# Kernel tuning notes

Measured on AMD Instinct MI355X. Metric: run time of the kernel, lower is better.

Reference implementation:

```python
import jax, jax.numpy as jnp
import numpy as np

N = 100000
E = 1600000
IN_C = 128
HID = 256
K_EIG = 64
OUT_C = 16


def setup_inputs() -> dict:
    key = jax.random.key(0)
    ks = jax.random.split(key, 8)
    x = jax.random.normal(ks[0], (N, IN_C), dtype=jnp.float32)
    edge_index = jax.random.randint(ks[1], (2, E), 0, N)
    MLP_W = jax.random.normal(ks[2], (K_EIG, N), dtype=jnp.float32) * 0.02
    MLP_b = jax.random.normal(ks[3], (K_EIG,), dtype=jnp.float32) * 0.02
    mlpx_W = jax.random.normal(ks[4], (HID, IN_C), dtype=jnp.float32) * 0.05
    mlpx_b = jax.random.normal(ks[5], (HID,), dtype=jnp.float32) * 0.02
    fin_W = jax.random.normal(ks[6], (OUT_C, HID + K_EIG), dtype=jnp.float32) * 0.05
    fin_b = jax.random.normal(ks[7], (OUT_C,), dtype=jnp.float32) * 0.02
    return {"x": x, "edge_index": edge_index, "MLP_W": MLP_W, "MLP_b": MLP_b,
            "mlpx_W": mlpx_W, "mlpx_b": mlpx_b, "fin_W": fin_W, "fin_b": fin_b}


def _spmm(row, col, feats, n):
    # adj is COO with coords (col[e], row[e]) and value 1 -> out[col] += feats[row]
    return jax.ops.segment_sum(feats[row], col, num_segments=n)


def _pump(xA, row, col, n):
    # MinCut-style pump: soft assignment, normalized-cut loss + orthogonality loss
    S = jax.nn.softmax(xA, axis=-1)                      # [N, K]
    AS = _spmm(row, col, S, n)                            # A @ S, [N, K]
    cut = jnp.sum(S * AS)                                 # tr(S^T A S)
    deg = jax.ops.segment_sum(jnp.ones(col.shape, S.dtype), col, num_segments=n)
    deg_term = jnp.sum(deg[:, None] * S * S)              # tr(S^T D S)
    pump_loss = -(cut / deg_term)
    SS = S.T @ S                                          # [K, K]
    k = S.shape[1]
    ortho_loss = jnp.linalg.norm(SS / jnp.linalg.norm(SS)
                                 - jnp.eye(k, dtype=S.dtype) / jnp.sqrt(jnp.asarray(k, S.dtype)))
    return S, pump_loss, ortho_loss


def reference(x, edge_index, MLP_W, MLP_b, mlpx_W, mlpx_b, fin_W, fin_b):
    row, col = edge_index[0], edge_index[1]
    n = x.shape[0]
    # xA = adj @ MLP.weight.T + bias   (irregular gather/scatter over edges)
    xA = _spmm(row, col, MLP_W.T, n) + MLP_b              # [N, K]
    xX = x @ mlpx_W.T + mlpx_b                            # [N, HID]
    xA, pump_loss, ortho_loss = _pump(xA, row, col, n)
    z = jnp.concatenate([xX, xA], axis=1)                 # [N, HID+K]
    # dropout omitted (eval mode)
    z = jax.nn.log_softmax(z @ fin_W.T + fin_b, axis=-1)  # [N, OUT]
    return (z, pump_loss + ortho_loss)
```

## Files before the change

### kernel.cpp

```cpp
#include <hip/hip_runtime.h>
#include <math.h>

#define N_NODES 100000
#define N_EDGES 1600000
#define IN_C    128
#define HID     256
#define KEIG    64
#define OUT_C   16

#define NPB      256
#define NBUCKET  ((N_NODES + NPB - 1) / NPB)
#define EDGE_TILE 2048
#define NTILE    ((N_EDGES + EDGE_TILE - 1) / EDGE_TILE)
#define CAP      8960

#define TRANS_BLOCKS   ((N_NODES + 63) / 64)
#define GATHER_BLOCKS  ((N_NODES + 63) / 64)
#define CUT_VB         1582
#define SSP_BLOCKS     226
#define SSP_ALLOC      256
#define OUTG_BLOCKS    226
#define TAIL_BLOCKS    (113 * 18)

typedef __attribute__((ext_vector_type(8))) short short8;
typedef __attribute__((ext_vector_type(4))) float f32x4;
typedef __attribute__((ext_vector_type(2))) float f32x2;

__device__ __forceinline__ float wave_sum(float v) {
#pragma unroll
    for (int m = 32; m; m >>= 1) v += __shfl_xor(v, m, 64);
    return v;
}
__device__ __forceinline__ float bf2f(unsigned int u) {
    return __uint_as_float((u & 0xffffu) << 16);
}
__device__ __forceinline__ unsigned short f2bf(float f) {
    unsigned int u = __float_as_uint(f);
    u += 0x7fff + ((u >> 16) & 1);
    return (unsigned short)(u >> 16);
}
__device__ __forceinline__ unsigned char f2fp8(float f) {
    int p = __builtin_amdgcn_cvt_pk_fp8_f32(f, f, 0, false);
    return (unsigned char)(p & 0xff);
}

#define FMA4(P, s, W) \
    P.x = fmaf(s, W.x, P.x); P.y = fmaf(s, W.y, P.y); \
    P.z = fmaf(s, W.z, P.z); P.w = fmaf(s, W.w, P.w);

#define GLD(TBL, R) (*(const unsigned*)((TBL) + (unsigned)(R) * 64u + cb))

#define CONS4(ACC) do { f32x2 p_;                                                   \
    p_ = __builtin_amdgcn_cvt_pk_f32_fp8(uA0, false); ACC.x += p_.x; ACC.y += p_.y; \
    p_ = __builtin_amdgcn_cvt_pk_f32_fp8(uA0, true);  ACC.z += p_.x; ACC.w += p_.y; \
    p_ = __builtin_amdgcn_cvt_pk_f32_fp8(uA1, false); ACC.x += p_.x; ACC.y += p_.y; \
    p_ = __builtin_amdgcn_cvt_pk_f32_fp8(uA1, true);  ACC.z += p_.x; ACC.w += p_.y; \
    p_ = __builtin_amdgcn_cvt_pk_f32_fp8(uA2, false); ACC.x += p_.x; ACC.y += p_.y; \
    p_ = __builtin_amdgcn_cvt_pk_f32_fp8(uA2, true);  ACC.z += p_.x; ACC.w += p_.y; \
    p_ = __builtin_amdgcn_cvt_pk_f32_fp8(uA3, false); ACC.x += p_.x; ACC.y += p_.y; \
    p_ = __builtin_amdgcn_cvt_pk_f32_fp8(uA3, true);  ACC.z += p_.x; ACC.w += p_.y; \
} while (0)

__global__ void prep_weff(const float* __restrict__ mlpxW, const float* __restrict__ mlpxb,
                          const float* __restrict__ finW, const float* __restrict__ finb,
                          float* __restrict__ Weff, float* __restrict__ beff,
                          int* __restrict__ bcnt, unsigned char* __restrict__ WT8,
                          unsigned char* __restrict__ S8, int* __restrict__ gpad) {
    int t = blockIdx.x * blockDim.x + threadIdx.x;
    const int NW = (IN_C + KEIG) * OUT_C;
    if (t < NW) {
        int k = t >> 4, o = t & 15;
        float acc;
        if (k < IN_C) {
            acc = 0.f;
            for (int c = 0; c < HID; ++c)
                acc += mlpxW[c * IN_C + k] * finW[o * (HID + KEIG) + c];
        } else {
            acc = finW[o * (HID + KEIG) + HID + (k - IN_C)];
        }
        Weff[k * OUT_C + o] = acc;
    }
    int tb = t - NW;
    if (tb >= 0 && tb < OUT_C) {
        float acc = finb[tb];
        for (int c = 0; c < HID; ++c) acc += mlpxb[c] * finW[tb * (HID + KEIG) + c];
        beff[tb] = acc;
    }
    int tz = t - (NW + OUT_C);
    if (tz >= 0 && tz <= NBUCKET) bcnt[tz] = 0;
    int tp = t - (NW + OUT_C + NBUCKET + 1);
    if (tp >= 0 && tp < 16) {
        ((int*)(WT8 + (size_t)N_NODES * 64))[tp] = 0;
        ((int*)(S8 + (size_t)N_NODES * 64))[tp] = 0;
        if (tp == 0) *gpad = 0;
    }
}

__global__ __launch_bounds__(256) void fused_prep(const float* __restrict__ W,
                                                  unsigned char* __restrict__ WT8,
                                                  const int* __restrict__ ei,
                                                  int* __restrict__ bcnt) {
    __shared__ __align__(16) char sm[64 * 65 * 4];
    int t = threadIdx.x;
    if (blockIdx.x < TRANS_BLOCKS) {
        float (*tile)[65] = (float (*)[65])sm;
        int n0 = blockIdx.x * 64;
        int tn = t & 63, tq = t >> 6;
#pragma unroll
        for (int kk = 0; kk < 16; ++kk) {
            int k = tq * 16 + kk;
            int n = n0 + tn;
            tile[k][tn] = (n < N_NODES) ? W[(long long)k * N_NODES + n] : 0.f;
        }
        __syncthreads();
        int tk = t & 63;
#pragma unroll
        for (int ii = 0; ii < 16; ++ii) {
            int n = n0 + tq * 16 + ii;
            if (n < N_NODES) WT8[(unsigned)n * 64u + tk] = f2fp8(tile[tk][tq * 16 + ii] * 32.f);
        }
    } else {
        int* h = (int*)sm;
        for (int i = t; i < NBUCKET; i += 256) h[i] = 0;
        __syncthreads();
        int tile_i = blockIdx.x - TRANS_BLOCKS;
        int e0 = tile_i * EDGE_TILE;
        int e1 = min(e0 + EDGE_TILE, N_EDGES);
        for (int e = e0 + t; e < e1; e += 256)
            atomicAdd(&h[ei[N_EDGES + e] >> 8], 1);
        __syncthreads();
        for (int i = t; i < NBUCKET; i += 256)
            if (h[i]) atomicAdd(&bcnt[i], h[i]);
    }
}

__global__ void bucket_scan(const int* __restrict__ bcnt, int* __restrict__ bbase,
                            int* __restrict__ bcur) {
    __shared__ int sh[512];
    int t = threadIdx.x;
    int v = (t < NBUCKET) ? bcnt[t] : 0;
    sh[t] = v;
    __syncthreads();
    for (int d = 1; d < 512; d <<= 1) {
        int u = (t >= d) ? sh[t - d] : 0;
        __syncthreads();
        sh[t] += u;
        __syncthreads();
    }
    if (t < NBUCKET) { bbase[t] = sh[t] - v; bcur[t] = sh[t] - v; }
    if (t == 0) bbase[NBUCKET] = N_EDGES;
}

__global__ void bucket_scatter(const int* __restrict__ ei, int* __restrict__ bcur,
                               int* __restrict__ ebuf) {
    __shared__ int h[NBUCKET];
    __shared__ int gb[NBUCKET];
    __shared__ int lpre[NBUCKET];
    __shared__ int psum[256];
    __shared__ int stage[EDGE_TILE];
    __shared__ short bkt[EDGE_TILE];
    int t = threadIdx.x;
    for (int i = t; i < NBUCKET; i += 256) h[i] = 0;
    __syncthreads();
    int e0 = blockIdx.x * EDGE_TILE;
    int e1 = min(e0 + EDGE_TILE, N_EDGES);
    int nt = e1 - e0;
    for (int e = e0 + t; e < e1; e += 256)
        atomicAdd(&h[ei[N_EDGES + e] >> 8], 1);
    __syncthreads();
    int a0 = (2 * t < NBUCKET) ? h[2 * t] : 0;
    int a1 = (2 * t + 1 < NBUCKET) ? h[2 * t + 1] : 0;
    psum[t] = a0 + a1;
    __syncthreads();
    for (int d = 1; d < 256; d <<= 1) {
        int u = (t >= d) ? psum[t - d] : 0;
        __syncthreads();
        psum[t] += u;
        __syncthreads();
    }
    int base = (t == 0) ? 0 : psum[t - 1];
    if (2 * t < NBUCKET) lpre[2 * t] = base;
    if (2 * t + 1 < NBUCKET) lpre[2 * t + 1] = base + a0;
    __syncthreads();
    for (int i = t; i < NBUCKET; i += 256) {
        int c = h[i];
        gb[i] = c ? atomicAdd(&bcur[i], c) : 0;
        h[i] = lpre[i];
    }
    __syncthreads();
    for (int e = e0 + t; e < e1; e += 256) {
        int r = ei[e];
        int c = ei[N_EDGES + e];
        int b = c >> 8;
        int slot = atomicAdd(&h[b], 1);
        stage[slot] = r | ((c & 255) << 17);
        bkt[slot] = (short)b;
    }
    __syncthreads();
    for (int s = t; s < nt; s += 256) {
        int b = bkt[s];
        ebuf[gb[b] + s - lpre[b]] = stage[s];
    }
}

__global__ void csr_build(const int* __restrict__ ebuf, const int* __restrict__ bbase,
                          int2* __restrict__ nodei,
                          int* __restrict__ csr_row, int* __restrict__ gpad) {
    __shared__ int hist[NPB];
    __shared__ int sh[NPB];
    __shared__ int curs[NPB];
    __shared__ int staged[CAP];
    __shared__ int pbase_sh;
    int b = blockIdx.x;
    int t = threadIdx.x;
    int s0 = bbase[b], s1 = bbase[b + 1];
    hist[t] = 0;
    __syncthreads();
    for (int i = s0 + t; i < s1; i += 256)
        atomicAdd(&hist[ebuf[i] >> 17], 1);
    __syncthreads();
    int v = hist[t];
    int pv = (v + 15) & ~15;
    sh[t] = pv;
    __syncthreads();
    for (int d = 1; d < 256; d <<= 1) {
        int u = (t >= d) ? sh[t - d] : 0;
        __syncthreads();
        sh[t] += u;
        __syncthreads();
    }
    int pexcl = sh[t] - pv;
    int pt = sh[255];
    if (t == 0) pbase_sh = atomicAdd(gpad, pt);
    __syncthreads();
    int pbase = pbase_sh;
    int node = b * NPB + t;
    if (node < N_NODES) nodei[node] = make_int2(v, pbase + pexcl);
    curs[t] = pexcl;
    __syncthreads();
    if (pt <= CAP) {
        for (int i = t; i < pt; i += 256) staged[i] = N_NODES;
        __syncthreads();
        for (int i = s0 + t; i < s1; i += 256) {
            int pk = ebuf[i];
            int pos = atomicAdd(&curs[pk >> 17], 1);
            staged[pos] = pk & 0x1FFFF;
        }
        __syncthreads();
        for (int i = t; i < pt; i += 256) csr_row[pbase + i] = staged[i];
    } else {
        for (int i = t; i < pt; i += 256) csr_row[pbase + i] = N_NODES;
        __syncthreads();
        for (int i = s0 + t; i < s1; i += 256) {
            int pk = ebuf[i];
            int pos = atomicAdd(&curs[pk >> 17], 1);
            csr_row[pbase + pos] = pk & 0x1FFFF;
        }
    }
}

__global__ __launch_bounds__(256, 4) void gather_softmax(
        const int2* __restrict__ nodei, const int* __restrict__ csr_row,
        const unsigned char* __restrict__ WT8, const float* __restrict__ MLPb,
        unsigned short* __restrict__ Sb, unsigned char* __restrict__ S8,
        float* __restrict__ dtp) {
    int lane = threadIdx.x & 63;
    int q = lane >> 4;
    int c = lane & 15;
    unsigned cb = (unsigned)c * 4u;
    int wib = __builtin_amdgcn_readfirstlane(threadIdx.x >> 6);
    int n0 = (blockIdx.x * 4 + wib) * 16;
    float dacc = 0.f;
    if (n0 < N_NODES) {
        int nvalid = min(16, N_NODES - n0);
        int2 di = nodei[n0 + min(c, nvalid - 1)];
        f32x4 bias = *(const f32x4*)(MLPb + c * 4);
        int ps0  = __shfl(di.y, 0, 64);
        int degL = __shfl(di.x, nvalid - 1, 64);
        int psL  = __shfl(di.y, nvalid - 1, 64);
        int G = ((psL + ((degL + 15) & ~15)) - ps0) >> 4;
        const int* cw = csr_row + ps0 + (q << 2);
        int4 iB = {0, 0, 0, 0};
        unsigned uA0 = 0, uA1 = 0, uA2 = 0, uA3 = 0;
        if (G > 0) {
            int4 iA = *(const int4*)(cw);
            uA0 = GLD(WT8, iA.x); uA1 = GLD(WT8, iA.y);
            uA2 = GLD(WT8, iA.z); uA3 = GLD(WT8, iA.w);
            int g1 = (G > 1) ? 1 : 0;
            iB = *(const int4*)(cw + (g1 << 4));
        }
        int g = 0;
        for (int k = 0; k < nvalid; ++k) {
            int deg = __shfl(di.x, k, 64);
            int gcnt = (deg + 15) >> 4;
            f32x4 acc = {0.f, 0.f, 0.f, 0.f};
            for (int tt = 0; tt < gcnt; ++tt) {
                int gn = g + 2; if (gn >= G) gn = G - 1;
                int4 iC = *(const int4*)(cw + (gn << 4));
                unsigned uB0 = GLD(WT8, iB.x);
                unsigned uB1 = GLD(WT8, iB.y);
                unsigned uB2 = GLD(WT8, iB.z);
                unsigned uB3 = GLD(WT8, iB.w);
                CONS4(acc);
                uA0 = uB0; uA1 = uB1; uA2 = uB2; uA3 = uB3; iB = iC;
                ++g;
            }
#pragma unroll
            for (int mm = 16; mm < 64; mm <<= 1) {
                acc.x += __shfl_xor(acc.x, mm, 64);
                acc.y += __shfl_xor(acc.y, mm, 64);
                acc.z += __shfl_xor(acc.z, mm, 64);
                acc.w += __shfl_xor(acc.w, mm, 64);
            }
            float ax = bias.x + acc.x * 0.03125f;
            float ay = bias.y + acc.y * 0.03125f;
            float az = bias.z + acc.z * 0.03125f;
            float aw = bias.w + acc.w * 0.03125f;
            float m4 = fmaxf(fmaxf(ax, ay), fmaxf(az, aw));
#pragma unroll
            for (int mm = 1; mm < 16; mm <<= 1) m4 = fmaxf(m4, __shfl_xor(m4, mm, 64));
            float ex = __expf(ax - m4), ey = __expf(ay - m4);
            float ez = __expf(az - m4), ew = __expf(aw - m4);
            float s4 = (ex + ey) + (ez + ew);
#pragma unroll
            for (int mm = 1; mm < 16; mm <<= 1) s4 += __shfl_xor(s4, mm, 64);
            float inv = 1.f / s4;
            float sx = ex * inv, sy = ey * inv, sz = ez * inv, sw = ew * inv;
            if (q == 0) {
                unsigned nidx = (unsigned)(n0 + k);
                unsigned lo = (unsigned)f2bf(sx) | ((unsigned)f2bf(sy) << 16);
                unsigned hi = (unsigned)f2bf(sz) | ((unsigned)f2bf(sw) << 16);
                *(uint2*)(Sb + nidx * 64u + cb) = make_uint2(lo, hi);
                int p8 = __builtin_amdgcn_cvt_pk_fp8_f32(sx * 64.f, sy * 64.f, 0, false);
                p8 = __builtin_amdgcn_cvt_pk_fp8_f32(sz * 64.f, sw * 64.f, p8, true);
                *(unsigned*)(S8 + nidx * 64u + cb) = (unsigned)p8;
            }
            dacc += (float)deg * ((sx * sx + sy * sy) + (sz * sz + sw * sw));
        }
    }
    dacc = wave_sum(dacc);
    __shared__ float red[4];
    if (lane == 0) red[wib] = dacc * 0.25f;
    __syncthreads();
    if (threadIdx.x == 0) dtp[blockIdx.x] = red[0] + red[1] + red[2] + red[3];
}

__global__ __launch_bounds__(256, 8) void fused_tail(
        const int2* __restrict__ nodei,
        const int* __restrict__ csr_row,
        const unsigned short* __restrict__ Sb, const unsigned char* __restrict__ S8,
        float* __restrict__ cutp, float* __restrict__ ssp,
        const float* __restrict__ x, const float* __restrict__ Weff,
        const float* __restrict__ beff, float* __restrict__ out) {
    __shared__ __align__(16) char sm[768 * 16 + 64];
    int t = threadIdx.x;
    int grp = blockIdx.x / 18;
    int r18 = blockIdx.x % 18;

    if (r18 < 14) {
        int vb = grp * 14 + r18;
        int lane = t & 63;
        int q = lane >> 4;
        int c = lane & 15;
        unsigned cb = (unsigned)c * 4u;
        int wib = __builtin_amdgcn_readfirstlane(t >> 6);
        int n0 = vb * 64 + wib * 16;
        float cacc = 0.f;
        if (n0 < N_NODES) {
            int nvalid = min(16, N_NODES - n0);
            int2 di = nodei[n0 + min(c, nvalid - 1)];
            int ps0  = __shfl(di.y, 0, 64);
            int degL = __shfl(di.x, nvalid - 1, 64);
            int psL  = __shfl(di.y, nvalid - 1, 64);
            int G = ((psL + ((degL + 15) & ~15)) - ps0) >> 4;
            const int* cw = csr_row + ps0 + (q << 2);
            uint2 suA = *(const uint2*)(Sb + (unsigned)n0 * 64u + cb);
            unsigned uA0 = 0, uA1 = 0, uA2 = 0, uA3 = 0;
            unsigned uB0 = 0, uB1 = 0, uB2 = 0, uB3 = 0;
            int4 iC = {0, 0, 0, 0};
            int4 iD = {0, 0, 0, 0};
            if (G > 0) {
                int4 i0 = *(const int4*)(cw);
                uA0 = GLD(S8, i0.x); uA1 = GLD(S8, i0.y);
                uA2 = GLD(S8, i0.z); uA3 = GLD(S8, i0.w);
                int g1 = (G > 1) ? 1 : G - 1;
                int4 i1 = *(const int4*)(cw + (g1 << 4));
                uB0 = GLD(S8, i1.x); uB1 = GLD(S8, i1.y);
                uB2 = GLD(S8, i1.z); uB3 = GLD(S8, i1.w);
                int g2 = (G > 2) ? 2 : G - 1;
                iC = *(const int4*)(cw + (g2 << 4));
                int g3 = (G > 3) ? 3 : G - 1;
                iD = *(const int4*)(cw + (g3 << 4));
            }
            int g = 0;
            for (int k = 0; k < nvalid; ++k) {
                int deg = __shfl(di.x, k, 64);
                int gcnt = (deg + 15) >> 4;
                uint2 suN = *(const uint2*)(Sb + (unsigned)(n0 + min(k + 1, nvalid - 1)) * 64u + cb);
                f32x4 acc = {0.f, 0.f, 0.f, 0.f};
                for (int tt = 0; tt < gcnt; ++tt) {
                    int gn = g + 4; if (gn >= G) gn = G - 1;
                    int4 iE_ = *(const int4*)(cw + (gn << 4));
                    unsigned uC0_ = GLD(S8, iC.x), uC1_ = GLD(S8, iC.y);
                    unsigned uC2_ = GLD(S8, iC.z), uC3_ = GLD(S8, iC.w);
                    CONS4(acc);
                    uA0 = uB0; uA1 = uB1; uA2 = uB2; uA3 = uB3;
                    uB0 = uC0_; uB1 = uC1_; uB2 = uC2_; uB3 = uC3_;
                    iC = iD; iD = iE_;
                    ++g;
                }
                cacc += bf2f(suA.x) * acc.x + bf2f(suA.x >> 16) * acc.y
                      + bf2f(suA.y) * acc.z + bf2f(suA.y >> 16) * acc.w;
                suA = suN;
            }
        }
        cacc = wave_sum(cacc);
        float* red = (float*)sm;
        if (lane == 0) red[wib] = cacc * 0.015625f;
        __syncthreads();
        if (t == 0) cutp[vb] = red[0] + red[1] + red[2] + red[3];
    } else if (r18 < 16) {
        int bid2 = grp * 2 + (r18 - 14);
        unsigned short (*Sr)[66] = (unsigned short (*)[66])sm;
        int lane = t & 63;
        int w = t >> 6;
        int m = lane & 15;
        int quad = lane >> 4;
        int srow = t >> 3;
        int spart = t & 7;
        f32x4 a0 = {0.f,0.f,0.f,0.f}, a1 = {0.f,0.f,0.f,0.f};
        f32x4 a2 = {0.f,0.f,0.f,0.f}, a3 = {0.f,0.f,0.f,0.f};
        for (int base = bid2 * 32; base < N_NODES; base += SSP_BLOCKS * 32) {
            const uint4* g = (const uint4*)(Sb + (long long)(base + srow) * 64 + spart * 8);
            uint4 d = *g;
            __syncthreads();
            unsigned int* rowp = (unsigned int*)&Sr[srow][0];
            rowp[spart * 4 + 0] = d.x;
            rowp[spart * 4 + 1] = d.y;
            rowp[spart * 4 + 2] = d.z;
            rowp[spart * 4 + 3] = d.w;
            __syncthreads();
            short8 f0, f1, f2, f3;
#pragma unroll
            for (int j = 0; j < 8; ++j) {
                int k = quad * 8 + j;
                f0[j] = (short)Sr[k][m];
                f1[j] = (short)Sr[k][16 + m];
                f2[j] = (short)Sr[k][32 + m];
                f3[j] = (short)Sr[k][48 + m];
            }
            short8 fa = (w == 0) ? f0 : (w == 1) ? f1 : (w == 2) ? f2 : f3;
            a0 = __builtin_amdgcn_mfma_f32_16x16x32_bf16(fa, f0, a0, 0, 0, 0);
            a1 = __builtin_amdgcn_mfma_f32_16x16x32_bf16(fa, f1, a1, 0, 0, 0);
            a2 = __builtin_amdgcn_mfma_f32_16x16x32_bf16(fa, f2, a2, 0, 0, 0);
            a3 = __builtin_amdgcn_mfma_f32_16x16x32_bf16(fa, f3, a3, 0, 0, 0);
        }
        float* dst = ssp + (size_t)bid2 * 4096;
#pragma unroll
        for (int r = 0; r < 4; ++r) {
            int row = w * 16 + quad * 4 + r;
            dst[row * 64 +  0 + m] = a0[r];
            dst[row * 64 + 16 + m] = a1[r];
            dst[row * 64 + 32 + m] = a2[r];
            dst[row * 64 + 48 + m] = a3[r];
        }
    } else {
        int obid = grp * 2 + (r18 - 16);
        float4* Wsh = (float4*)sm;
        float* bsh = (float*)(sm + 768 * 16);
        const float4* W4 = (const float4*)Weff;
        for (int i = t; i < 768; i += 256) Wsh[i] = W4[i];
        if (t < 16) bsh[t] = beff[t];
        __syncthreads();
        for (int r = obid * 256 + t; r < N_NODES; r += OUTG_BLOCKS * 256) {
            float4 p0 = make_float4(bsh[0], bsh[1], bsh[2], bsh[3]);
            float4 p1 = make_float4(bsh[4], bsh[5], bsh[6], bsh[7]);
            float4 p2 = make_float4(bsh[8], bsh[9], bsh[10], bsh[11]);
            float4 p3 = make_float4(bsh[12], bsh[13], bsh[14], bsh[15]);
            const float4* xr = (const float4*)(x + (long long)r * IN_C);
#pragma unroll 8
            for (int j = 0; j < 32; ++j) {
                float4 xv = xr[j];
                int k = j * 4;
                float xs[4] = {xv.x, xv.y, xv.z, xv.w};
#pragma unroll
                for (int c = 0; c < 4; ++c) {
                    float s = xs[c];
                    float4 w0 = Wsh[(k + c) * 4 + 0];
                    float4 w1 = Wsh[(k + c) * 4 + 1];
                    float4 w2 = Wsh[(k + c) * 4 + 2];
                    float4 w3 = Wsh[(k + c) * 4 + 3];
                    FMA4(p0, s, w0); FMA4(p1, s, w1); FMA4(p2, s, w2); FMA4(p3, s, w3);
                }
            }
            const uint2* sr = (const uint2*)(Sb + (long long)r * 64);
#pragma unroll 8
            for (int j = 0; j < 16; ++j) {
                uint2 u = sr[j];
                float xs[4] = {bf2f(u.x), bf2f(u.x >> 16), bf2f(u.y), bf2f(u.y >> 16)};
                int k = IN_C + j * 4;
#pragma unroll
                for (int c = 0; c < 4; ++c) {
                    float s = xs[c];
                    float4 w0 = Wsh[(k + c) * 4 + 0];
                    float4 w1 = Wsh[(k + c) * 4 + 1];
                    float4 w2 = Wsh[(k + c) * 4 + 2];
                    float4 w3 = Wsh[(k + c) * 4 + 3];
                    FMA4(p0, s, w0); FMA4(p1, s, w1); FMA4(p2, s, w2); FMA4(p3, s, w3);
                }
            }
            float m = fmaxf(fmaxf(fmaxf(p0.x, p0.y), fmaxf(p0.z, p0.w)),
                            fmaxf(fmaxf(fmaxf(p1.x, p1.y), fmaxf(p1.z, p1.w)),
                                  fmaxf(fmaxf(fmaxf(p2.x, p2.y), fmaxf(p2.z, p2.w)),
                                        fmaxf(fmaxf(p3.x, p3.y), fmaxf(p3.z, p3.w)))));
            float sum = __expf(p0.x - m) + __expf(p0.y - m) + __expf(p0.z - m) + __expf(p0.w - m)
                      + __expf(p1.x - m) + __expf(p1.y - m) + __expf(p1.z - m) + __expf(p1.w - m)
                      + __expf(p2.x - m) + __expf(p2.y - m) + __expf(p2.z - m) + __expf(p2.w - m)
                      + __expf(p3.x - m) + __expf(p3.y - m) + __expf(p3.z - m) + __expf(p3.w - m);
            float lse = m + logf(sum);
            float4* o4 = (float4*)(out + (long long)r * OUT_C);
            o4[0] = make_float4(p0.x - lse, p0.y - lse, p0.z - lse, p0.w - lse);
            o4[1] = make_float4(p1.x - lse, p1.y - lse, p1.z - lse, p1.w - lse);
            o4[2] = make_float4(p2.x - lse, p2.y - lse, p2.z - lse, p2.w - lse);
            o4[3] = make_float4(p3.x - lse, p3.y - lse, p3.z - lse, p3.w - lse);
        }
    }
}

__global__ void reduce_ss(const float* __restrict__ ssp, float* __restrict__ SS) {
    int e = blockIdx.x * blockDim.x + threadIdx.x;
    float s = 0.f;
    for (int p = 0; p < SSP_BLOCKS; ++p) s += ssp[(size_t)p * 4096 + e];
    SS[e] = s;
}

__global__ void scalars_kernel(const float* __restrict__ cutp, const float* __restrict__ dtp,
                               const float* __restrict__ SS, float* __restrict__ out) {
    __shared__ float red[256];
    int t = threadIdx.x;
    float c = 0.f;
    for (int i = t; i < CUT_VB; i += 256) c += cutp[i];
    red[t] = c; __syncthreads();
    for (int s = 128; s; s >>= 1) { if (t < s) red[t] += red[t + s]; __syncthreads(); }
    float cut = red[0]; __syncthreads();

    float d = 0.f;
    for (int i = t; i < GATHER_BLOCKS; i += 256) d += dtp[i];
    red[t] = d; __syncthreads();
    for (int s = 128; s; s >>= 1) { if (t < s) red[t] += red[t + s]; __syncthreads(); }
    float dterm = red[0]; __syncthreads();

    float ss[16];
    float sq = 0.f;
#pragma unroll
    for (int j = 0; j < 16; ++j) { ss[j] = SS[t * 16 + j]; sq += ss[j] * ss[j]; }
    red[t] = sq; __syncthreads();
    for (int s = 128; s; s >>= 1) { if (t < s) red[t] += red[t + s]; __syncthreads(); }
    float nrm = sqrtf(red[0]); __syncthreads();

    float osq = 0.f;
#pragma unroll
    for (int j = 0; j < 16; ++j) {
        int idx = t * 16 + j;
        float v = ss[j] / nrm - ((idx % 65 == 0) ? 0.125f : 0.f);
        osq += v * v;
    }
    red[t] = osq; __syncthreads();
    for (int s = 128; s; s >>= 1) { if (t < s) red[t] += red[t + s]; __syncthreads(); }
    if (t == 0) {
        float loss = -(cut / dterm) + sqrtf(red[0]);
        out[(long long)N_NODES * OUT_C] = loss;
    }
}

extern "C" void kernel_launch(void* const* d_in, const int* in_sizes, int n_in,
                              void* d_out, int out_size, void* d_ws, size_t ws_size,
                              hipStream_t stream) {
    const float* x     = (const float*)d_in[0];
    const int*   ei    = (const int*)d_in[1];
    const float* MLPW  = (const float*)d_in[2];
    const float* MLPb  = (const float*)d_in[3];
    const float* mlpxW = (const float*)d_in[4];
    const float* mlpxb = (const float*)d_in[5];
    const float* finW  = (const float*)d_in[6];
    const float* finb  = (const float*)d_in[7];
    float* out = (float*)d_out;
    char* ws = (char*)d_ws;

    unsigned char*  WT8 = (unsigned char*)ws;
    unsigned char*  S8  = (unsigned char*)(ws + (size_t)(N_NODES + 1) * 64);
    unsigned short* Sb  = (unsigned short*)(ws + (size_t)(N_NODES + 1) * 128);
    char* p = ws + (size_t)(N_NODES + 1) * 128 + (size_t)N_NODES * 128;
    float* ssp  = (float*)p;
    float* SS   = ssp + (size_t)SSP_ALLOC * 4096;
    float* Weff = SS + 4096;
    float* beff = Weff + 192 * 16;
    float* cutp = beff + 16;
    float* dtp  = cutp + 2048;
    int* ebuf    = (int*)(dtp + 2048);
    int* csr_row = ebuf + N_EDGES;
    int2* nodei  = (int2*)(csr_row + N_EDGES + 16 * N_NODES);
    int* bcnt    = (int*)(nodei + N_NODES);
    int* bbase   = bcnt + NBUCKET + 1;
    int* bcur    = bbase + NBUCKET + 1;
    int* gpad    = bcur + NBUCKET;

    hipLaunchKernelGGL(prep_weff, dim3(16), dim3(256), 0, stream,
                       mlpxW, mlpxb, finW, finb, Weff, beff, bcnt, WT8, S8, gpad);
    hipLaunchKernelGGL(fused_prep, dim3(TRANS_BLOCKS + NTILE), dim3(256), 0, stream,
                       MLPW, WT8, ei, bcnt);
    hipLaunchKernelGGL(bucket_scan, dim3(1), dim3(512), 0, stream, bcnt, bbase, bcur);
    hipLaunchKernelGGL(bucket_scatter, dim3(NTILE), dim3(256), 0, stream, ei, bcur, ebuf);
    hipLaunchKernelGGL(csr_build, dim3(NBUCKET), dim3(256), 0, stream,
                       ebuf, bbase, nodei, csr_row, gpad);
    hipLaunchKernelGGL(gather_softmax, dim3(GATHER_BLOCKS), dim3(256), 0, stream,
                       nodei, csr_row, WT8, MLPb, Sb, S8, dtp);
    hipLaunchKernelGGL(fused_tail, dim3(TAIL_BLOCKS), dim3(256), 0, stream,
                       nodei, csr_row, Sb, S8, cutp, ssp, x, Weff, beff, out);
    hipLaunchKernelGGL(reduce_ss, dim3(16), dim3(256), 0, stream, ssp, SS);
    hipLaunchKernelGGL(scalars_kernel, dim3(1), dim3(256), 0, stream, cutp, dtp, SS, out);
}
```

Before: 324.3 us.

## Fuse CSR build with gather-softmax, halve bucket size, read indices from LDS

Merges the CSR construction kernel and the gather+softmax kernel into one per-bucket kernel. The padded row indices staged in shared memory are reused directly for the WT8 gather instead of being reread from global memory. Buckets shrink from 256 to 128 nodes so the staging array fits within the occupancy bound, and the scan and scatter kernels are resized to match. This removes one launch and the global reread of csr_row, at the cost of giving up the cross-node software prefetch pipeline and possibly leaving less parallelism per block.

```diff
diff --git a/kernel.cpp b/kernel.cpp
--- a/kernel.cpp
+++ b/kernel.cpp
@@ -8,14 +8,13 @@
 #define KEIG    64
 #define OUT_C   16
 
-#define NPB      256
+#define NPB      128
 #define NBUCKET  ((N_NODES + NPB - 1) / NPB)
 #define EDGE_TILE 2048
 #define NTILE    ((N_EDGES + EDGE_TILE - 1) / EDGE_TILE)
-#define CAP      8960
+#define CAP      4608
 
 #define TRANS_BLOCKS   ((N_NODES + 63) / 64)
-#define GATHER_BLOCKS  ((N_NODES + 63) / 64)
 #define CUT_VB         1582
 #define SSP_BLOCKS     226
 #define SSP_ALLOC      256
@@ -59,6 +58,20 @@
     p_ = __builtin_amdgcn_cvt_pk_f32_fp8(uA2, true);  ACC.z += p_.x; ACC.w += p_.y; \
     p_ = __builtin_amdgcn_cvt_pk_f32_fp8(uA3, false); ACC.x += p_.x; ACC.y += p_.y; \
     p_ = __builtin_amdgcn_cvt_pk_f32_fp8(uA3, true);  ACC.z += p_.x; ACC.w += p_.y; \
+} while (0)
+
+#define GS_GATHER(IDX4, ACC) do {                                                   \
+    int4 ii_ = IDX4(0);                                                             \
+    unsigned uA0 = GLD(WT8, ii_.x), uA1 = GLD(WT8, ii_.y);                          \
+    unsigned uA2 = GLD(WT8, ii_.z), uA3 = GLD(WT8, ii_.w);                          \
+    for (int j_ = 16; j_ < plen; j_ += 16) {                                        \
+        int4 jj_ = IDX4(j_);                                                        \
+        unsigned uB0 = GLD(WT8, jj_.x), uB1 = GLD(WT8, jj_.y);                      \
+        unsigned uB2 = GLD(WT8, jj_.z), uB3 = GLD(WT8, jj_.w);                      \
+        CONS4(ACC);                                                                 \
+        uA0 = uB0; uA1 = uB1; uA2 = uB2; uA3 = uB3;                                 \
+    }                                                                               \
+    CONS4(ACC);                                                                     \
 } while (0)
 
 __global__ void prep_weff(const float* __restrict__ mlpxW, const float* __restrict__ mlpxb,
@@ -127,7 +140,7 @@
         int e0 = tile_i * EDGE_TILE;
         int e1 = min(e0 + EDGE_TILE, N_EDGES);
         for (int e = e0 + t; e < e1; e += 256)
-            atomicAdd(&h[ei[N_EDGES + e] >> 8], 1);
+            atomicAdd(&h[ei[N_EDGES + e] >> 7], 1);
         __syncthreads();
         for (int i = t; i < NBUCKET; i += 256)
             if (h[i]) atomicAdd(&bcnt[i], h[i]);
@@ -136,12 +149,12 @@
 
 __global__ void bucket_scan(const int* __restrict__ bcnt, int* __restrict__ bbase,
                             int* __restrict__ bcur) {
-    __shared__ int sh[512];
+    __shared__ int sh[1024];
     int t = threadIdx.x;
     int v = (t < NBUCKET) ? bcnt[t] : 0;
     sh[t] = v;
     __syncthreads();
-    for (int d = 1; d < 512; d <<= 1) {
+    for (int d = 1; d < 1024; d <<= 1) {
         int u = (t >= d) ? sh[t - d] : 0;
         __syncthreads();
         sh[t] += u;
@@ -166,11 +179,13 @@
     int e1 = min(e0 + EDGE_TILE, N_EDGES);
     int nt = e1 - e0;
     for (int e = e0 + t; e < e1; e += 256)
-        atomicAdd(&h[ei[N_EDGES + e] >> 8], 1);
-    __syncthreads();
-    int a0 = (2 * t < NBUCKET) ? h[2 * t] : 0;
-    int a1 = (2 * t + 1 < NBUCKET) ? h[2 * t + 1] : 0;
-    psum[t] = a0 + a1;
+        atomicAdd(&h[ei[N_EDGES + e] >> 7], 1);
+    __syncthreads();
+    int a0 = (4 * t + 0 < NBUCKET) ? h[4 * t + 0] : 0;
+    int a1 = (4 * t + 1 < NBUCKET) ? h[4 * t + 1] : 0;
+    int a2 = (4 * t + 2 < NBUCKET) ? h[4 * t + 2] : 0;
+    int a3 = (4 * t + 3 < NBUCKET) ? h[4 * t + 3] : 0;
+    psum[t] = a0 + a1 + a2 + a3;
     __syncthreads();
     for (int d = 1; d < 256; d <<= 1) {
         int u = (t >= d) ? psum[t - d] : 0;
@@ -179,8 +194,10 @@
         __syncthreads();
     }
     int base = (t == 0) ? 0 : psum[t - 1];
-    if (2 * t < NBUCKET) lpre[2 * t] = base;
-    if (2 * t + 1 < NBUCKET) lpre[2 * t + 1] = base + a0;
+    if (4 * t + 0 < NBUCKET) lpre[4 * t + 0] = base;
+    if (4 * t + 1 < NBUCKET) lpre[4 * t + 1] = base + a0;
+    if (4 * t + 2 < NBUCKET) lpre[4 * t + 2] = base + a0 + a1;
+    if (4 * t + 3 < NBUCKET) lpre[4 * t + 3] = base + a0 + a1 + a2;
     __syncthreads();
     for (int i = t; i < NBUCKET; i += 256) {
         int c = h[i];
@@ -191,9 +208,9 @@
     for (int e = e0 + t; e < e1; e += 256) {
         int r = ei[e];
         int c = ei[N_EDGES + e];
-        int b = c >> 8;
+        int b = c >> 7;
         int slot = atomicAdd(&h[b], 1);
-        stage[slot] = r | ((c & 255) << 17);
+        stage[slot] = r | ((c & 127) << 17);
         bkt[slot] = (short)b;
     }
     __syncthreads();
@@ -203,42 +220,50 @@
     }
 }
 
-__global__ void csr_build(const int* __restrict__ ebuf, const int* __restrict__ bbase,
-                          int2* __restrict__ nodei,
-                          int* __restrict__ csr_row, int* __restrict__ gpad) {
+__global__ __launch_bounds__(256, 4) void build_gather(
+        const int* __restrict__ ebuf, const int* __restrict__ bbase,
+        int2* __restrict__ nodei, int* __restrict__ csr_row, int* __restrict__ gpad,
+        const unsigned char* __restrict__ WT8, const float* __restrict__ MLPb,
+        unsigned short* __restrict__ Sb, unsigned char* __restrict__ S8,
+        float* __restrict__ dtp) {
     __shared__ int hist[NPB];
-    __shared__ int sh[NPB];
+    __shared__ int shh[NPB];
+    __shared__ int pstartL[NPB];
     __shared__ int curs[NPB];
     __shared__ int staged[CAP];
     __shared__ int pbase_sh;
+    __shared__ float red[4];
     int b = blockIdx.x;
     int t = threadIdx.x;
     int s0 = bbase[b], s1 = bbase[b + 1];
-    hist[t] = 0;
+    if (t < NPB) hist[t] = 0;
     __syncthreads();
     for (int i = s0 + t; i < s1; i += 256)
         atomicAdd(&hist[ebuf[i] >> 17], 1);
     __syncthreads();
-    int v = hist[t];
-    int pv = (v + 15) & ~15;
-    sh[t] = pv;
-    __syncthreads();
-    for (int d = 1; d < 256; d <<= 1) {
-        int u = (t >= d) ? sh[t - d] : 0;
-        __syncthreads();
-        sh[t] += u;
-        __syncthreads();
-    }
-    int pexcl = sh[t] - pv;
-    int pt = sh[255];
+    int v = 0, pv = 0;
+    if (t < NPB) { v = hist[t]; pv = (v + 15) & ~15; shh[t] = pv; }
+    __syncthreads();
+    for (int d = 1; d < NPB; d <<= 1) {
+        int u = (t < NPB && t >= d) ? shh[t - d] : 0;
+        __syncthreads();
+        if (t < NPB) shh[t] += u;
+        __syncthreads();
+    }
+    int pt = shh[NPB - 1];
     if (t == 0) pbase_sh = atomicAdd(gpad, pt);
     __syncthreads();
     int pbase = pbase_sh;
-    int node = b * NPB + t;
-    if (node < N_NODES) nodei[node] = make_int2(v, pbase + pexcl);
-    curs[t] = pexcl;
-    __syncthreads();
-    if (pt <= CAP) {
+    if (t < NPB) {
+        int pexcl = shh[t] - pv;
+        pstartL[t] = pexcl;
+        curs[t] = pexcl;
+        int node = b * NPB + t;
+        if (node < N_NODES) nodei[node] = make_int2(v, pbase + pexcl);
+    }
+    __syncthreads();
+    bool fit = (pt <= CAP);
+    if (fit) {
         for (int i = t; i < pt; i += 256) staged[i] = N_NODES;
         __syncthreads();
         for (int i = s0 + t; i < s1; i += 256) {
@@ -256,93 +281,68 @@
             int pos = atomicAdd(&curs[pk >> 17], 1);
             csr_row[pbase + pos] = pk & 0x1FFFF;
         }
-    }
-}
-
-__global__ __launch_bounds__(256, 4) void gather_softmax(
-        const int2* __restrict__ nodei, const int* __restrict__ csr_row,
-        const unsigned char* __restrict__ WT8, const float* __restrict__ MLPb,
-        unsigned short* __restrict__ Sb, unsigned char* __restrict__ S8,
-        float* __restrict__ dtp) {
-    int lane = threadIdx.x & 63;
+        __threadfence();
+    }
+    __syncthreads();
+    int lane = t & 63;
     int q = lane >> 4;
     int c = lane & 15;
     unsigned cb = (unsigned)c * 4u;
-    int wib = __builtin_amdgcn_readfirstlane(threadIdx.x >> 6);
-    int n0 = (blockIdx.x * 4 + wib) * 16;
+    int w = __builtin_amdgcn_readfirstlane(t >> 6);
+    f32x4 bias = *(const f32x4*)(MLPb + c * 4);
     float dacc = 0.f;
-    if (n0 < N_NODES) {
-        int nvalid = min(16, N_NODES - n0);
-        int2 di = nodei[n0 + min(c, nvalid - 1)];
-        f32x4 bias = *(const f32x4*)(MLPb + c * 4);
-        int ps0  = __shfl(di.y, 0, 64);
-        int degL = __shfl(di.x, nvalid - 1, 64);
-        int psL  = __shfl(di.y, nvalid - 1, 64);
-        int G = ((psL + ((degL + 15) & ~15)) - ps0) >> 4;
-        const int* cw = csr_row + ps0 + (q << 2);
-        int4 iB = {0, 0, 0, 0};
-        unsigned uA0 = 0, uA1 = 0, uA2 = 0, uA3 = 0;
-        if (G > 0) {
-            int4 iA = *(const int4*)(cw);
-            uA0 = GLD(WT8, iA.x); uA1 = GLD(WT8, iA.y);
-            uA2 = GLD(WT8, iA.z); uA3 = GLD(WT8, iA.w);
-            int g1 = (G > 1) ? 1 : 0;
-            iB = *(const int4*)(cw + (g1 << 4));
-        }
-        int g = 0;
-        for (int k = 0; k < nvalid; ++k) {
-            int deg = __shfl(di.x, k, 64);
-            int gcnt = (deg + 15) >> 4;
-            f32x4 acc = {0.f, 0.f, 0.f, 0.f};
-            for (int tt = 0; tt < gcnt; ++tt) {
-                int gn = g + 2; if (gn >= G) gn = G - 1;
-                int4 iC = *(const int4*)(cw + (gn << 4));
-                unsigned uB0 = GLD(WT8, iB.x);
-                unsigned uB1 = GLD(WT8, iB.y);
-                unsigned uB2 = GLD(WT8, iB.z);
-                unsigned uB3 = GLD(WT8, iB.w);
-                CONS4(acc);
-                uA0 = uB0; uA1 = uB1; uA2 = uB2; uA3 = uB3; iB = iC;
-                ++g;
-            }
-#pragma unroll
-            for (int mm = 16; mm < 64; mm <<= 1) {
-                acc.x += __shfl_xor(acc.x, mm, 64);
-                acc.y += __shfl_xor(acc.y, mm, 64);
-                acc.z += __shfl_xor(acc.z, mm, 64);
-                acc.w += __shfl_xor(acc.w, mm, 64);
-            }
-            float ax = bias.x + acc.x * 0.03125f;
-            float ay = bias.y + acc.y * 0.03125f;
-            float az = bias.z + acc.z * 0.03125f;
-            float aw = bias.w + acc.w * 0.03125f;
-            float m4 = fmaxf(fmaxf(ax, ay), fmaxf(az, aw));
-#pragma unroll
-            for (int mm = 1; mm < 16; mm <<= 1) m4 = fmaxf(m4, __shfl_xor(m4, mm, 64));
-            float ex = __expf(ax - m4), ey = __expf(ay - m4);
-            float ez = __expf(az - m4), ew = __expf(aw - m4);
-            float s4 = (ex + ey) + (ez + ew);
-#pragma unroll
-            for (int mm = 1; mm < 16; mm <<= 1) s4 += __shfl_xor(s4, mm, 64);
-            float inv = 1.f / s4;
-            float sx = ex * inv, sy = ey * inv, sz = ez * inv, sw = ew * inv;
-            if (q == 0) {
-                unsigned nidx = (unsigned)(n0 + k);
-                unsigned lo = (unsigned)f2bf(sx) | ((unsigned)f2bf(sy) << 16);
-                unsigned hi = (unsigned)f2bf(sz) | ((unsigned)f2bf(sw) << 16);
-                *(uint2*)(Sb + nidx * 64u + cb) = make_uint2(lo, hi);
-                int p8 = __builtin_amdgcn_cvt_pk_fp8_f32(sx * 64.f, sy * 64.f, 0, false);
-                p8 = __builtin_amdgcn_cvt_pk_fp8_f32(sz * 64.f, sw * 64.f, p8, true);
-                *(unsigned*)(S8 + nidx * 64u + cb) = (unsigned)p8;
-            }
-            dacc += (float)deg * ((sx * sx + sy * sy) + (sz * sz + sw * sw));
-        }
-    }
+    int k0 = w * 32;
+#define IDX_LDS(J)  (*(const int4*)&staged[ps + (J) + (q << 2)])
+#define IDX_GBL(J)  (*(const int4*)&csr_row[pbase + ps + (J) + (q << 2)])
+    for (int k = k0; k < k0 + 32; ++k) {
+        int n = b * NPB + k;
+        if (n >= N_NODES) break;
+        int deg = hist[k];
+        int ps  = pstartL[k];
+        int plen = (deg + 15) & ~15;
+        f32x4 acc = {0.f, 0.f, 0.f, 0.f};
+        if (plen > 0) {
+            if (fit) { GS_GATHER(IDX_LDS, acc); }
+            else     { GS_GATHER(IDX_GBL, acc); }
+        }
+#pragma unroll
+        for (int mm = 16; mm < 64; mm <<= 1) {
+            acc.x += __shfl_xor(acc.x, mm, 64);
+            acc.y += __shfl_xor(acc.y, mm, 64);
+            acc.z += __shfl_xor(acc.z, mm, 64);
+            acc.w += __shfl_xor(acc.w, mm, 64);
+        }
+        float ax = bias.x + acc.x * 0.03125f;
+        float ay = bias.y + acc.y * 0.03125f;
+        float az = bias.z + acc.z * 0.03125f;
+        float aw = bias.w + acc.w * 0.03125f;
+        float m4 = fmaxf(fmaxf(ax, ay), fmaxf(az, aw));
+#pragma unroll
+        for (int mm = 1; mm < 16; mm <<= 1) m4 = fmaxf(m4, __shfl_xor(m4, mm, 64));
+        float ex = __expf(ax - m4), ey = __expf(ay - m4);
+        float ez = __expf(az - m4), ew = __expf(aw - m4);
+        float s4 = (ex + ey) + (ez + ew);
+#pragma unroll
+        for (int mm = 1; mm < 16; mm <<= 1) s4 += __shfl_xor(s4, mm, 64);
+        float inv = 1.f / s4;
+        float sx = ex * inv, sy = ey * inv, sz = ez * inv, sw = ew * inv;
+        if (q == 0) {
+            unsigned nidx = (unsigned)n;
+            unsigned lo = (unsigned)f2bf(sx) | ((unsigned)f2bf(sy) << 16);
+            unsigned hi = (unsigned)f2bf(sz) | ((unsigned)f2bf(sw) << 16);
+            *(uint2*)(Sb + nidx * 64u + cb) = make_uint2(lo, hi);
+            int p8 = __builtin_amdgcn_cvt_pk_fp8_f32(sx * 64.f, sy * 64.f, 0, false);
+            p8 = __builtin_amdgcn_cvt_pk_fp8_f32(sz * 64.f, sw * 64.f, p8, true);
+            *(unsigned*)(S8 + nidx * 64u + cb) = (unsigned)p8;
+        }
+        dacc += (float)deg * ((sx * sx + sy * sy) + (sz * sz + sw * sw));
+    }
+#undef IDX_LDS
+#undef IDX_GBL
     dacc = wave_sum(dacc);
-    __shared__ float red[4];
-    if (lane == 0) red[wib] = dacc * 0.25f;
-    __syncthreads();
-    if (threadIdx.x == 0) dtp[blockIdx.x] = red[0] + red[1] + red[2] + red[3];
+    if (lane == 0) red[w] = dacc * 0.25f;
+    __syncthreads();
+    if (t == 0) dtp[b] = red[0] + red[1] + red[2] + red[3];
 }
 
 __global__ __launch_bounds__(256, 8) void fused_tail(
@@ -545,7 +545,7 @@
     float cut = red[0]; __syncthreads();
 
     float d = 0.f;
-    for (int i = t; i < GATHER_BLOCKS; i += 256) d += dtp[i];
+    for (int i = t; i < NBUCKET; i += 256) d += dtp[i];
     red[t] = d; __syncthreads();
     for (int s = 128; s; s >>= 1) { if (t < s) red[t] += red[t + s]; __syncthreads(); }
     float dterm = red[0]; __syncthreads();
@@ -609,12 +609,10 @@
                        mlpxW, mlpxb, finW, finb, Weff, beff, bcnt, WT8, S8, gpad);
     hipLaunchKernelGGL(fused_prep, dim3(TRANS_BLOCKS + NTILE), dim3(256), 0, stream,
                        MLPW, WT8, ei, bcnt);
-    hipLaunchKernelGGL(bucket_scan, dim3(1), dim3(512), 0, stream, bcnt, bbase, bcur);
+    hipLaunchKernelGGL(bucket_scan, dim3(1), dim3(1024), 0, stream, bcnt, bbase, bcur);
     hipLaunchKernelGGL(bucket_scatter, dim3(NTILE), dim3(256), 0, stream, ei, bcur, ebuf);
-    hipLaunchKernelGGL(csr_build, dim3(NBUCKET), dim3(256), 0, stream,
-                       ebuf, bbase, nodei, csr_row, gpad);
-    hipLaunchKernelGGL(gather_softmax, dim3(GATHER_BLOCKS), dim3(256), 0, stream,
-                       nodei, csr_row, WT8, MLPb, Sb, S8, dtp);
+    hipLaunchKernelGGL(build_gather, dim3(NBUCKET), dim3(256), 0, stream,
+                       ebuf, bbase, nodei, csr_row, gpad, WT8, MLPb, Sb, S8, dtp);
     hipLaunchKernelGGL(fused_tail, dim3(TAIL_BLOCKS), dim3(256), 0, stream,
                        nodei, csr_row, Sb, S8, cutp, ssp, x, Weff, beff, out);
     hipLaunchKernelGGL(reduce_ss, dim3(16), dim3(256), 0, stream, ssp, SS);
```

Result: slower. 348.8 us (+7.6%).
